# Optimization experiments

Hardware: AMD Instinct MI355X
Metric: run time of the kernel (lower is better)

Reference implementation:

```python
import jax, jax.numpy as jnp
import numpy as np
import math

ALPHA = 0.25
GAMMA = 2.0
STD = np.array([0.1, 0.1, 0.2, 0.2], dtype=np.float32).reshape(4, 1)


def setup_inputs() -> dict:
    rng = np.random.default_rng(0)
    B, C, Na, Nb = 8, 80, 49104, 64
    cls_pred = rng.uniform(0.01, 0.99, (B, C, Na)).astype(np.float32)
    reg_pred = (0.5 * rng.standard_normal((B, 4, Na))).astype(np.float32)
    # anchors in x1,y1,x2,y2 with positive width/height
    cx = rng.uniform(0.0, 512.0, Na); cy = rng.uniform(0.0, 512.0, Na)
    w = rng.uniform(16.0, 128.0, Na); h = rng.uniform(16.0, 128.0, Na)
    anchors = np.stack([cx - 0.5 * w, cy - 0.5 * h, cx + 0.5 * w, cy + 0.5 * h], 1).astype(np.float32)
    # annotations: valid boxes first, padded with label=-1
    x1 = rng.uniform(0.0, 380.0, (B, Nb)); y1 = rng.uniform(0.0, 380.0, (B, Nb))
    bw = rng.uniform(24.0, 120.0, (B, Nb)); bh = rng.uniform(24.0, 120.0, (B, Nb))
    lab = rng.integers(0, C, (B, Nb)).astype(np.float32)
    nvalid = rng.integers(1, Nb + 1, B)
    valid = np.arange(Nb)[None, :] < nvalid[:, None]
    lab = np.where(valid, lab, -1.0)
    annots = np.stack([x1, y1, x1 + bw, y1 + bh, lab], -1).astype(np.float32)
    return {"cls_pred": jnp.asarray(cls_pred), "reg_pred": jnp.asarray(reg_pred),
            "annots": jnp.asarray(annots), "anchors": jnp.asarray(anchors)}


def _focal(pred, targets):
    alpha_f = jnp.where(targets == 1.0, ALPHA, 1.0 - ALPHA)
    fw = jnp.where(targets == 1.0, 1.0 - pred, pred)
    bce = -(targets * jnp.log(pred) + (1.0 - targets) * jnp.log(1.0 - pred))
    return alpha_f * fw ** GAMMA * bce


def _ciou(acx, acy, aw, ah, gcx, gcy, gw, gh, reg):
    # acx/acy/aw/ah: [1,Na]; gt: [B,Na]; reg: [B,4,Na] (std-scaled)
    pcx = acx + reg[:, 0] * aw
    pcy = acy + reg[:, 1] * ah
    pw = jnp.exp(reg[:, 2]) * aw
    ph = jnp.exp(reg[:, 3]) * ah
    g_area = gw * gh
    p_area = pw * ph
    ix1 = jnp.maximum(gcx - 0.5 * gw, pcx - 0.5 * pw)
    ix2 = jnp.minimum(gcx + 0.5 * gw, pcx + 0.5 * pw)
    iy1 = jnp.maximum(gcy - 0.5 * gh, pcy - 0.5 * ph)
    iy2 = jnp.minimum(gcy + 0.5 * gh, pcy + 0.5 * ph)
    inter = jnp.clip(ix2 - ix1, 0.0) * jnp.clip(iy2 - iy1, 0.0)
    ex1 = jnp.minimum(gcx - 0.5 * gw, pcx - 0.5 * pw)
    ex2 = jnp.maximum(gcx + 0.5 * gw, pcx + 0.5 * pw)
    ey1 = jnp.minimum(gcy - 0.5 * gh, pcy - 0.5 * ph)
    ey2 = jnp.maximum(gcy + 0.5 * gh, pcy + 0.5 * ph)
    inter_diag = (gcx - pcx) ** 2 + (gcy - pcy) ** 2
    enc_diag = jnp.clip(ex2 - ex1, 0.0) ** 2 + jnp.clip(ey2 - ey1, 0.0) ** 2
    union = g_area + p_area - inter
    u = inter_diag / jnp.clip(enc_diag, 1e-6)
    iou = inter / jnp.clip(union, 1e-6)
    v = (4.0 / math.pi ** 2) * (jnp.arctan(gw / gh) - jnp.arctan(pw / ph)) ** 2
    S = (iou > 0.5).astype(iou.dtype)
    alpha = jax.lax.stop_gradient(S * v / jnp.clip(1.0 - iou + v, 1e-6))
    ciou = jnp.clip(iou - u - alpha * v, -1.0, 1.0)
    return 1.0 - ciou


def _multibox_loss(cls_pred, reg_pred, annots, anchors):
    reg = reg_pred * jnp.asarray(STD)[None]            # [B,4,Na]
    aw = anchors[:, 2] - anchors[:, 0]
    ah = anchors[:, 3] - anchors[:, 1]
    acx = anchors[:, 0] + 0.5 * aw
    acy = anchors[:, 1] + 0.5 * ah
    cls = jnp.clip(cls_pred, 1e-7, 1.0 - 1e-7)         # [B,C,Na]
    valid = annots[:, :, 4] != -1.0                    # [B,Nb]
    boxes = annots[:, :, :4]
    # dense IoU [B,Na,Nb]
    a = anchors[None, :, None, :]
    bx = boxes[:, None, :, :]
    a_area = aw * ah                                   # [Na]
    b_area = (boxes[..., 2] - boxes[..., 0]) * (boxes[..., 3] - boxes[..., 1])
    iw = jnp.clip(jnp.minimum(a[..., 2], bx[..., 2]) - jnp.maximum(a[..., 0], bx[..., 0]), 0.0)
    ih = jnp.clip(jnp.minimum(a[..., 3], bx[..., 3]) - jnp.maximum(a[..., 1], bx[..., 1]), 0.0)
    inter = iw * ih
    union = jnp.clip(a_area[None, :, None] + b_area[:, None, :] - inter, 1e-7)
    iou = inter / union
    iou = jnp.where(valid[:, None, :], iou, -1.0)      # mask padded boxes
    iou_max = iou.max(-1)                              # [B,Na]
    iou_arg = iou.argmax(-1)                           # [B,Na]
    has_boxes = valid.any(-1)                          # [B]
    pos = (iou_max >= 0.5) & has_boxes[:, None]        # [B,Na]
    assigned = jnp.take_along_axis(annots, iou_arg[..., None], axis=1)  # [B,Na,5]
    labels = assigned[..., 4].astype(jnp.int32)
    C = cls.shape[1]
    posf = pos.astype(cls.dtype)
    targets = jax.nn.one_hot(labels, C, dtype=cls.dtype) * posf[..., None]
    targets = jnp.transpose(targets, (0, 2, 1))        # [B,C,Na]
    num_pos = posf.sum(-1)                             # [B]
    cls_loss = _focal(cls, targets).sum((1, 2)) / jnp.clip(num_pos, 1.0)
    gw = jnp.clip(assigned[..., 2] - assigned[..., 0], 1.0)
    gh = jnp.clip(assigned[..., 3] - assigned[..., 1], 1.0)
    gcx = assigned[..., 0] + 0.5 * gw
    gcy = assigned[..., 1] + 0.5 * gh
    ciou = _ciou(acx[None], acy[None], aw[None], ah[None], gcx, gcy, gw, gh, reg)  # [B,Na]
    reg_loss = (ciou * posf).sum(-1) / jnp.clip(num_pos, 1.0)
    reg_loss = jnp.where(num_pos > 0, reg_loss, 0.0)
    return cls_loss.mean(), reg_loss.mean()


def reference(cls_pred, reg_pred, annots, anchors):
    return _multibox_loss(cls_pred, reg_pred, annots, anchors)
```

## Files before the change

### kernel.cpp

```cpp
#include <hip/hip_runtime.h>
#include <math.h>

#define NB_MAX 64
#define CCHUNK 10


__global__ __launch_bounds__(256) void assign_kernel(
    const float* __restrict__ reg_pred,
    const float* __restrict__ annots,
    const float* __restrict__ anchors,
    signed char* __restrict__ labels,
    float* __restrict__ reg_part,
    float* __restrict__ pos_part,
    int Na, int Nb, int nblkA)
{
    int b = blockIdx.y;
    int a = blockIdx.x * 256 + threadIdx.x;

    __shared__ float ann[NB_MAX][5];
    const float* ab = annots + b * Nb * 5;
    for (int i = threadIdx.x; i < Nb * 5; i += 256) ann[i / 5][i % 5] = ab[i];
    __syncthreads();

    float regv = 0.f, posv = 0.f;
    if (a < Na) {
        float4 anc = ((const float4*)anchors)[a];
        float ax1 = anc.x, ay1 = anc.y, ax2 = anc.z, ay2 = anc.w;
        float aw = ax2 - ax1, ah = ay2 - ay1;
        float a_area = aw * ah;

        float best = -1.f; int bestj = 0;
        for (int j = 0; j < Nb; ++j) {
            float lab = ann[j][4];
            float iou = -1.0f;
            if (lab != -1.0f) {
                float bx1 = ann[j][0], by1 = ann[j][1], bx2 = ann[j][2], by2 = ann[j][3];
                float iw = fmaxf(fminf(ax2, bx2) - fmaxf(ax1, bx1), 0.f);
                float ih = fmaxf(fminf(ay2, by2) - fmaxf(ay1, by1), 0.f);
                float inter = iw * ih;
                float b_area = (bx2 - bx1) * (by2 - by1);
                float un = fmaxf(a_area + b_area - inter, 1e-7f);
                iou = inter / un;
            }
            if (iou > best) { best = iou; bestj = j; }
        }

        signed char lout = -1;
        if (best >= 0.5f) {
            lout = (signed char)(int)ann[bestj][4];

            float r0 = reg_pred[(size_t)(b * 4 + 0) * Na + a] * 0.1f;
            float r1 = reg_pred[(size_t)(b * 4 + 1) * Na + a] * 0.1f;
            float r2 = reg_pred[(size_t)(b * 4 + 2) * Na + a] * 0.2f;
            float r3 = reg_pred[(size_t)(b * 4 + 3) * Na + a] * 0.2f;

            float acx = ax1 + 0.5f * aw, acy = ay1 + 0.5f * ah;
            float pcx = acx + r0 * aw;
            float pcy = acy + r1 * ah;
            float pw = expf(r2) * aw;
            float ph = expf(r3) * ah;

            float g0 = ann[bestj][0], g1 = ann[bestj][1];
            float g2 = ann[bestj][2], g3 = ann[bestj][3];
            float gw = fmaxf(g2 - g0, 1.0f);
            float gh = fmaxf(g3 - g1, 1.0f);
            float gcx = g0 + 0.5f * gw;
            float gcy = g1 + 0.5f * gh;

            float g_area = gw * gh, p_area = pw * ph;
            float ix1 = fmaxf(gcx - 0.5f * gw, pcx - 0.5f * pw);
            float ix2 = fminf(gcx + 0.5f * gw, pcx + 0.5f * pw);
            float iy1 = fmaxf(gcy - 0.5f * gh, pcy - 0.5f * ph);
            float iy2 = fminf(gcy + 0.5f * gh, pcy + 0.5f * ph);
            float inter = fmaxf(ix2 - ix1, 0.f) * fmaxf(iy2 - iy1, 0.f);

            float ex1 = fminf(gcx - 0.5f * gw, pcx - 0.5f * pw);
            float ex2 = fmaxf(gcx + 0.5f * gw, pcx + 0.5f * pw);
            float ey1 = fminf(gcy - 0.5f * gh, pcy - 0.5f * ph);
            float ey2 = fmaxf(gcy + 0.5f * gh, pcy + 0.5f * ph);

            float dx = gcx - pcx, dy = gcy - pcy;
            float inter_diag = dx * dx + dy * dy;
            float cdx = fmaxf(ex2 - ex1, 0.f), cdy = fmaxf(ey2 - ey1, 0.f);
            float enc_diag = cdx * cdx + cdy * cdy;

            float uni = g_area + p_area - inter;
            float u = inter_diag / fmaxf(enc_diag, 1e-6f);
            float iou = inter / fmaxf(uni, 1e-6f);
            float dv = atanf(gw / gh) - atanf(pw / ph);
            float v = (4.0f / (float)(M_PI * M_PI)) * dv * dv;
            float S = (iou > 0.5f) ? 1.f : 0.f;
            float alpha = S * v / fmaxf(1.f - iou + v, 1e-6f);
            float ciou = fminf(fmaxf(iou - u - alpha * v, -1.f), 1.f);
            regv = 1.f - ciou;
            posv = 1.f;
        }
        labels[(size_t)b * Na + a] = lout;
    }

    __shared__ float s1[4], s2[4];
    #pragma unroll
    for (int off = 32; off > 0; off >>= 1) {
        regv += __shfl_down(regv, off);
        posv += __shfl_down(posv, off);
    }
    int lane = threadIdx.x & 63, wid = threadIdx.x >> 6;
    if (lane == 0) { s1[wid] = regv; s2[wid] = posv; }
    __syncthreads();
    if (threadIdx.x == 0) {
        reg_part[(size_t)b * nblkA + blockIdx.x] = s1[0] + s1[1] + s1[2] + s1[3];
        pos_part[(size_t)b * nblkA + blockIdx.x] = s2[0] + s2[1] + s2[2] + s2[3];
    }
}

__device__ __forceinline__ float focal1(float p, bool t) {
    p = fminf(fmaxf(p, 1e-7f), 0.99999988f);
    float q = t ? p : 1.0f - p;
    float af = t ? 0.25f : 0.75f;
    float fw = 1.0f - q;
    return af * fw * fw * (-__logf(q));
}

__global__ __launch_bounds__(256) void focal_kernel(
    const float* __restrict__ cls_pred,
    const signed char* __restrict__ labels,
    float* __restrict__ cls_part,
    int Na, int C, int nchunk, int nblkF)
{
    int b = blockIdx.z;
    int No = Na >> 3;
    int Nq = Na >> 2;
    int q = blockIdx.x * 256 + threadIdx.x;
    int c0 = blockIdx.y * CCHUNK;
    int cend = min(c0 + CCHUNK, C);

    float sum = 0.f;
    if (q < No) {
        const char4* lp = (const char4*)(labels + (size_t)b * Na) + 2 * q;
        char4 la = lp[0], lb = lp[1];
        int l0 = la.x, l1 = la.y, l2 = la.z, l3 = la.w;
        int l4 = lb.x, l5 = lb.y, l6 = lb.z, l7 = lb.w;
        const float4* base = (const float4*)cls_pred + (size_t)b * C * Nq + 2 * q;
        for (int c = c0; c < cend; ++c) {
            float4 p0 = base[(size_t)c * Nq];
            float4 p1 = base[(size_t)c * Nq + 1];
            sum += focal1(p0.x, l0 == c);
            sum += focal1(p0.y, l1 == c);
            sum += focal1(p0.z, l2 == c);
            sum += focal1(p0.w, l3 == c);
            sum += focal1(p1.x, l4 == c);
            sum += focal1(p1.y, l5 == c);
            sum += focal1(p1.z, l6 == c);
            sum += focal1(p1.w, l7 == c);
        }
    }

    __shared__ float s[4];
    #pragma unroll
    for (int off = 32; off > 0; off >>= 1) sum += __shfl_down(sum, off);
    int lane = threadIdx.x & 63, wid = threadIdx.x >> 6;
    if (lane == 0) s[wid] = sum;
    __syncthreads();
    if (threadIdx.x == 0) {
        cls_part[(size_t)b * nblkF + blockIdx.x * nchunk + blockIdx.y] =
            s[0] + s[1] + s[2] + s[3];
    }
}

__global__ __launch_bounds__(512) void finalize_kernel(
    const float* __restrict__ reg_part,
    const float* __restrict__ pos_part,
    const float* __restrict__ cls_part,
    float* __restrict__ out,
    int B, int nblkA, int nblkF)
{
    int w = threadIdx.x >> 6;
    int lane = threadIdx.x & 63;

    float cs = 0.f, rs = 0.f, ps = 0.f;
    if (w < B) {
        for (int i = lane; i < nblkA; i += 64) {
            rs += reg_part[(size_t)w * nblkA + i];
            ps += pos_part[(size_t)w * nblkA + i];
        }
        for (int i = lane; i < nblkF; i += 64) {
            cs += cls_part[(size_t)w * nblkF + i];
        }
    }
    #pragma unroll
    for (int off = 32; off > 0; off >>= 1) {
        cs += __shfl_down(cs, off);
        rs += __shfl_down(rs, off);
        ps += __shfl_down(ps, off);
    }
    __shared__ float sc[8], sr[8];
    if (w < B && lane == 0) {
        float d = fmaxf(ps, 1.f);
        sc[w] = cs / d;
        sr[w] = (ps > 0.f) ? rs / d : 0.f;
    }
    __syncthreads();
    if (threadIdx.x == 0) {
        float a = 0.f, r = 0.f;
        for (int i = 0; i < B; ++i) { a += sc[i]; r += sr[i]; }
        out[0] = a / (float)B;
        out[1] = r / (float)B;
    }
}

extern "C" void kernel_launch(void* const* d_in, const int* in_sizes, int n_in,
                              void* d_out, int out_size, void* d_ws, size_t ws_size,
                              hipStream_t stream) {
    const float* cls     = (const float*)d_in[0];
    const float* reg     = (const float*)d_in[1];
    const float* annots  = (const float*)d_in[2];
    const float* anchors = (const float*)d_in[3];

    int Na = in_sizes[3] / 4;
    int B  = in_sizes[1] / (4 * Na);
    int C  = in_sizes[0] / (B * Na);
    int Nb = in_sizes[2] / (B * 5);

    int nblkA  = (Na + 255) / 256;
    int No     = Na / 8;
    int nblkX  = (No + 255) / 256;
    int nchunk = (C + CCHUNK - 1) / CCHUNK;
    int nblkF  = nblkX * nchunk;

    signed char* labels = (signed char*)d_ws;
    size_t off = ((size_t)B * Na + 255) & ~(size_t)255;
    float* reg_part = (float*)((char*)d_ws + off);
    float* pos_part = reg_part + (size_t)B * nblkA;
    float* cls_part = pos_part + (size_t)B * nblkA;
    float* out = (float*)d_out;

    dim3 g1(nblkA, B);
    assign_kernel<<<g1, 256, 0, stream>>>(reg, annots, anchors, labels,
                                          reg_part, pos_part, Na, Nb, nblkA);

    dim3 g2(nblkX, nchunk, B);
    focal_kernel<<<g2, 256, 0, stream>>>(cls, labels, cls_part, Na, C, nchunk, nblkF);

    finalize_kernel<<<1, 512, 0, stream>>>(reg_part, pos_part, cls_part, out,
                                           B, nblkA, nblkF);
}
```

Before: 210.7 us.

## Fuse anchor assignment and focal loss into a single kernel

Merges the assignment/CIoU kernel and the focal-loss kernel into one. Each thread handles two anchors, computes their labels in registers and then streams all C classes of cls_pred as float2. This removes the int8 label round-trip through global memory and one kernel launch. In exchange the grid shrinks to about 96 blocks per batch (about 770 total), each looping over all 80 classes. The Nb-long IoU search also runs serially before the memory-bound loop, which may lower occupancy and memory-level parallelism.

```diff
diff --git a/kernel.cpp b/kernel.cpp
--- a/kernel.cpp
+++ b/kernel.cpp
@@ -2,116 +2,7 @@
 #include <math.h>
 
 #define NB_MAX 64
-#define CCHUNK 10
-
-
-__global__ __launch_bounds__(256) void assign_kernel(
-    const float* __restrict__ reg_pred,
-    const float* __restrict__ annots,
-    const float* __restrict__ anchors,
-    signed char* __restrict__ labels,
-    float* __restrict__ reg_part,
-    float* __restrict__ pos_part,
-    int Na, int Nb, int nblkA)
-{
-    int b = blockIdx.y;
-    int a = blockIdx.x * 256 + threadIdx.x;
-
-    __shared__ float ann[NB_MAX][5];
-    const float* ab = annots + b * Nb * 5;
-    for (int i = threadIdx.x; i < Nb * 5; i += 256) ann[i / 5][i % 5] = ab[i];
-    __syncthreads();
-
-    float regv = 0.f, posv = 0.f;
-    if (a < Na) {
-        float4 anc = ((const float4*)anchors)[a];
-        float ax1 = anc.x, ay1 = anc.y, ax2 = anc.z, ay2 = anc.w;
-        float aw = ax2 - ax1, ah = ay2 - ay1;
-        float a_area = aw * ah;
-
-        float best = -1.f; int bestj = 0;
-        for (int j = 0; j < Nb; ++j) {
-            float lab = ann[j][4];
-            float iou = -1.0f;
-            if (lab != -1.0f) {
-                float bx1 = ann[j][0], by1 = ann[j][1], bx2 = ann[j][2], by2 = ann[j][3];
-                float iw = fmaxf(fminf(ax2, bx2) - fmaxf(ax1, bx1), 0.f);
-                float ih = fmaxf(fminf(ay2, by2) - fmaxf(ay1, by1), 0.f);
-                float inter = iw * ih;
-                float b_area = (bx2 - bx1) * (by2 - by1);
-                float un = fmaxf(a_area + b_area - inter, 1e-7f);
-                iou = inter / un;
-            }
-            if (iou > best) { best = iou; bestj = j; }
-        }
-
-        signed char lout = -1;
-        if (best >= 0.5f) {
-            lout = (signed char)(int)ann[bestj][4];
-
-            float r0 = reg_pred[(size_t)(b * 4 + 0) * Na + a] * 0.1f;
-            float r1 = reg_pred[(size_t)(b * 4 + 1) * Na + a] * 0.1f;
-            float r2 = reg_pred[(size_t)(b * 4 + 2) * Na + a] * 0.2f;
-            float r3 = reg_pred[(size_t)(b * 4 + 3) * Na + a] * 0.2f;
-
-            float acx = ax1 + 0.5f * aw, acy = ay1 + 0.5f * ah;
-            float pcx = acx + r0 * aw;
-            float pcy = acy + r1 * ah;
-            float pw = expf(r2) * aw;
-            float ph = expf(r3) * ah;
-
-            float g0 = ann[bestj][0], g1 = ann[bestj][1];
-            float g2 = ann[bestj][2], g3 = ann[bestj][3];
-            float gw = fmaxf(g2 - g0, 1.0f);
-            float gh = fmaxf(g3 - g1, 1.0f);
-            float gcx = g0 + 0.5f * gw;
-            float gcy = g1 + 0.5f * gh;
-
-            float g_area = gw * gh, p_area = pw * ph;
-            float ix1 = fmaxf(gcx - 0.5f * gw, pcx - 0.5f * pw);
-            float ix2 = fminf(gcx + 0.5f * gw, pcx + 0.5f * pw);
-            float iy1 = fmaxf(gcy - 0.5f * gh, pcy - 0.5f * ph);
-            float iy2 = fminf(gcy + 0.5f * gh, pcy + 0.5f * ph);
-            float inter = fmaxf(ix2 - ix1, 0.f) * fmaxf(iy2 - iy1, 0.f);
-
-            float ex1 = fminf(gcx - 0.5f * gw, pcx - 0.5f * pw);
-            float ex2 = fmaxf(gcx + 0.5f * gw, pcx + 0.5f * pw);
-            float ey1 = fminf(gcy - 0.5f * gh, pcy - 0.5f * ph);
-            float ey2 = fmaxf(gcy + 0.5f * gh, pcy + 0.5f * ph);
-
-            float dx = gcx - pcx, dy = gcy - pcy;
-            float inter_diag = dx * dx + dy * dy;
-            float cdx = fmaxf(ex2 - ex1, 0.f), cdy = fmaxf(ey2 - ey1, 0.f);
-            float enc_diag = cdx * cdx + cdy * cdy;
-
-            float uni = g_area + p_area - inter;
-            float u = inter_diag / fmaxf(enc_diag, 1e-6f);
-            float iou = inter / fmaxf(uni, 1e-6f);
-            float dv = atanf(gw / gh) - atanf(pw / ph);
-            float v = (4.0f / (float)(M_PI * M_PI)) * dv * dv;
-            float S = (iou > 0.5f) ? 1.f : 0.f;
-            float alpha = S * v / fmaxf(1.f - iou + v, 1e-6f);
-            float ciou = fminf(fmaxf(iou - u - alpha * v, -1.f), 1.f);
-            regv = 1.f - ciou;
-            posv = 1.f;
-        }
-        labels[(size_t)b * Na + a] = lout;
-    }
-
-    __shared__ float s1[4], s2[4];
-    #pragma unroll
-    for (int off = 32; off > 0; off >>= 1) {
-        regv += __shfl_down(regv, off);
-        posv += __shfl_down(posv, off);
-    }
-    int lane = threadIdx.x & 63, wid = threadIdx.x >> 6;
-    if (lane == 0) { s1[wid] = regv; s2[wid] = posv; }
-    __syncthreads();
-    if (threadIdx.x == 0) {
-        reg_part[(size_t)b * nblkA + blockIdx.x] = s1[0] + s1[1] + s1[2] + s1[3];
-        pos_part[(size_t)b * nblkA + blockIdx.x] = s2[0] + s2[1] + s2[2] + s2[3];
-    }
-}
+
 
 __device__ __forceinline__ float focal1(float p, bool t) {
     p = fminf(fmaxf(p, 1e-7f), 0.99999988f);
@@ -121,70 +12,149 @@
     return af * fw * fw * (-__logf(q));
 }
 
-__global__ __launch_bounds__(256) void focal_kernel(
+__global__ __launch_bounds__(256) void fused_kernel(
     const float* __restrict__ cls_pred,
-    const signed char* __restrict__ labels,
+    const float* __restrict__ reg_pred,
+    const float* __restrict__ annots,
+    const float* __restrict__ anchors,
     float* __restrict__ cls_part,
-    int Na, int C, int nchunk, int nblkF)
+    float* __restrict__ reg_part,
+    float* __restrict__ pos_part,
+    int Na, int Nb, int C, int nblk)
 {
-    int b = blockIdx.z;
-    int No = Na >> 3;
-    int Nq = Na >> 2;
-    int q = blockIdx.x * 256 + threadIdx.x;
-    int c0 = blockIdx.y * CCHUNK;
-    int cend = min(c0 + CCHUNK, C);
-
-    float sum = 0.f;
-    if (q < No) {
-        const char4* lp = (const char4*)(labels + (size_t)b * Na) + 2 * q;
-        char4 la = lp[0], lb = lp[1];
-        int l0 = la.x, l1 = la.y, l2 = la.z, l3 = la.w;
-        int l4 = lb.x, l5 = lb.y, l6 = lb.z, l7 = lb.w;
-        const float4* base = (const float4*)cls_pred + (size_t)b * C * Nq + 2 * q;
-        for (int c = c0; c < cend; ++c) {
-            float4 p0 = base[(size_t)c * Nq];
-            float4 p1 = base[(size_t)c * Nq + 1];
-            sum += focal1(p0.x, l0 == c);
-            sum += focal1(p0.y, l1 == c);
-            sum += focal1(p0.z, l2 == c);
-            sum += focal1(p0.w, l3 == c);
-            sum += focal1(p1.x, l4 == c);
-            sum += focal1(p1.y, l5 == c);
-            sum += focal1(p1.z, l6 == c);
-            sum += focal1(p1.w, l7 == c);
+    int b = blockIdx.y;
+    int h = blockIdx.x * 256 + threadIdx.x;
+    int Nh = Na >> 1;
+
+    __shared__ float ann[NB_MAX][5];
+    const float* ab = annots + b * Nb * 5;
+    for (int i = threadIdx.x; i < Nb * 5; i += 256) ann[i / 5][i % 5] = ab[i];
+    __syncthreads();
+
+    float clsv = 0.f, regv = 0.f, posv = 0.f;
+    int lab[2] = {-1, -1};
+
+    if (h < Nh) {
+        #pragma unroll
+        for (int s = 0; s < 2; ++s) {
+            int a = 2 * h + s;
+            float4 anc = ((const float4*)anchors)[a];
+            float ax1 = anc.x, ay1 = anc.y, ax2 = anc.z, ay2 = anc.w;
+            float aw = ax2 - ax1, ah = ay2 - ay1;
+            float a_area = aw * ah;
+
+            float best = -1.f; int bestj = 0;
+            for (int j = 0; j < Nb; ++j) {
+                float labj = ann[j][4];
+                float iou = -1.0f;
+                if (labj != -1.0f) {
+                    float bx1 = ann[j][0], by1 = ann[j][1];
+                    float bx2 = ann[j][2], by2 = ann[j][3];
+                    float iw = fmaxf(fminf(ax2, bx2) - fmaxf(ax1, bx1), 0.f);
+                    float ih = fmaxf(fminf(ay2, by2) - fmaxf(ay1, by1), 0.f);
+                    float inter = iw * ih;
+                    float b_area = (bx2 - bx1) * (by2 - by1);
+                    float un = fmaxf(a_area + b_area - inter, 1e-7f);
+                    iou = inter / un;
+                }
+                if (iou > best) { best = iou; bestj = j; }
+            }
+
+            if (best >= 0.5f) {
+                lab[s] = (int)ann[bestj][4];
+
+                float r0 = reg_pred[(size_t)(b * 4 + 0) * Na + a] * 0.1f;
+                float r1 = reg_pred[(size_t)(b * 4 + 1) * Na + a] * 0.1f;
+                float r2 = reg_pred[(size_t)(b * 4 + 2) * Na + a] * 0.2f;
+                float r3 = reg_pred[(size_t)(b * 4 + 3) * Na + a] * 0.2f;
+
+                float acx = ax1 + 0.5f * aw, acy = ay1 + 0.5f * ah;
+                float pcx = acx + r0 * aw;
+                float pcy = acy + r1 * ah;
+                float pw = expf(r2) * aw;
+                float ph = expf(r3) * ah;
+
+                float g0 = ann[bestj][0], g1 = ann[bestj][1];
+                float g2 = ann[bestj][2], g3 = ann[bestj][3];
+                float gw = fmaxf(g2 - g0, 1.0f);
+                float gh = fmaxf(g3 - g1, 1.0f);
+                float gcx = g0 + 0.5f * gw;
+                float gcy = g1 + 0.5f * gh;
+
+                float g_area = gw * gh, p_area = pw * ph;
+                float ix1 = fmaxf(gcx - 0.5f * gw, pcx - 0.5f * pw);
+                float ix2 = fminf(gcx + 0.5f * gw, pcx + 0.5f * pw);
+                float iy1 = fmaxf(gcy - 0.5f * gh, pcy - 0.5f * ph);
+                float iy2 = fminf(gcy + 0.5f * gh, pcy + 0.5f * ph);
+                float inter = fmaxf(ix2 - ix1, 0.f) * fmaxf(iy2 - iy1, 0.f);
+
+                float ex1 = fminf(gcx - 0.5f * gw, pcx - 0.5f * pw);
+                float ex2 = fmaxf(gcx + 0.5f * gw, pcx + 0.5f * pw);
+                float ey1 = fminf(gcy - 0.5f * gh, pcy - 0.5f * ph);
+                float ey2 = fmaxf(gcy + 0.5f * gh, pcy + 0.5f * ph);
+
+                float dx = gcx - pcx, dy = gcy - pcy;
+                float inter_diag = dx * dx + dy * dy;
+                float cdx = fmaxf(ex2 - ex1, 0.f), cdy = fmaxf(ey2 - ey1, 0.f);
+                float enc_diag = cdx * cdx + cdy * cdy;
+
+                float uni = g_area + p_area - inter;
+                float u = inter_diag / fmaxf(enc_diag, 1e-6f);
+                float iou = inter / fmaxf(uni, 1e-6f);
+                float dv = atanf(gw / gh) - atanf(pw / ph);
+                float v = (4.0f / (float)(M_PI * M_PI)) * dv * dv;
+                float S = (iou > 0.5f) ? 1.f : 0.f;
+                float alpha = S * v / fmaxf(1.f - iou + v, 1e-6f);
+                float ciou = fminf(fmaxf(iou - u - alpha * v, -1.f), 1.f);
+                regv += 1.f - ciou;
+                posv += 1.f;
+            }
         }
-    }
-
-    __shared__ float s[4];
+
+        int l0 = lab[0], l1 = lab[1];
+        const float2* base = (const float2*)cls_pred + (size_t)b * C * Nh + h;
+        #pragma unroll 4
+        for (int c = 0; c < C; ++c) {
+            float2 p = base[(size_t)c * Nh];
+            clsv += focal1(p.x, l0 == c);
+            clsv += focal1(p.y, l1 == c);
+        }
+    }
+
+    __shared__ float s1[4], s2[4], s3[4];
     #pragma unroll
-    for (int off = 32; off > 0; off >>= 1) sum += __shfl_down(sum, off);
+    for (int off = 32; off > 0; off >>= 1) {
+        clsv += __shfl_down(clsv, off);
+        regv += __shfl_down(regv, off);
+        posv += __shfl_down(posv, off);
+    }
     int lane = threadIdx.x & 63, wid = threadIdx.x >> 6;
-    if (lane == 0) s[wid] = sum;
+    if (lane == 0) { s1[wid] = clsv; s2[wid] = regv; s3[wid] = posv; }
     __syncthreads();
     if (threadIdx.x == 0) {
-        cls_part[(size_t)b * nblkF + blockIdx.x * nchunk + blockIdx.y] =
-            s[0] + s[1] + s[2] + s[3];
+        size_t slot = (size_t)b * nblk + blockIdx.x;
+        cls_part[slot] = s1[0] + s1[1] + s1[2] + s1[3];
+        reg_part[slot] = s2[0] + s2[1] + s2[2] + s2[3];
+        pos_part[slot] = s3[0] + s3[1] + s3[2] + s3[3];
     }
 }
 
 __global__ __launch_bounds__(512) void finalize_kernel(
+    const float* __restrict__ cls_part,
     const float* __restrict__ reg_part,
     const float* __restrict__ pos_part,
-    const float* __restrict__ cls_part,
     float* __restrict__ out,
-    int B, int nblkA, int nblkF)
+    int B, int nblk)
 {
     int w = threadIdx.x >> 6;
     int lane = threadIdx.x & 63;
 
     float cs = 0.f, rs = 0.f, ps = 0.f;
     if (w < B) {
-        for (int i = lane; i < nblkA; i += 64) {
-            rs += reg_part[(size_t)w * nblkA + i];
-            ps += pos_part[(size_t)w * nblkA + i];
-        }
-        for (int i = lane; i < nblkF; i += 64) {
-            cs += cls_part[(size_t)w * nblkF + i];
+        for (int i = lane; i < nblk; i += 64) {
+            cs += cls_part[(size_t)w * nblk + i];
+            rs += reg_part[(size_t)w * nblk + i];
+            ps += pos_part[(size_t)w * nblk + i];
         }
     }
     #pragma unroll
@@ -221,26 +191,19 @@
     int C  = in_sizes[0] / (B * Na);
     int Nb = in_sizes[2] / (B * 5);
 
-    int nblkA  = (Na + 255) / 256;
-    int No     = Na / 8;
-    int nblkX  = (No + 255) / 256;
-    int nchunk = (C + CCHUNK - 1) / CCHUNK;
-    int nblkF  = nblkX * nchunk;
-
-    signed char* labels = (signed char*)d_ws;
-    size_t off = ((size_t)B * Na + 255) & ~(size_t)255;
-    float* reg_part = (float*)((char*)d_ws + off);
-    float* pos_part = reg_part + (size_t)B * nblkA;
-    float* cls_part = pos_part + (size_t)B * nblkA;
+    int Nh   = Na / 2;
+    int nblk = (Nh + 255) / 256;
+
+    float* cls_part = (float*)d_ws;
+    float* reg_part = cls_part + (size_t)B * nblk;
+    float* pos_part = reg_part + (size_t)B * nblk;
     float* out = (float*)d_out;
 
-    dim3 g1(nblkA, B);
-    assign_kernel<<<g1, 256, 0, stream>>>(reg, annots, anchors, labels,
-                                          reg_part, pos_part, Na, Nb, nblkA);
-
-    dim3 g2(nblkX, nchunk, B);
-    focal_kernel<<<g2, 256, 0, stream>>>(cls, labels, cls_part, Na, C, nchunk, nblkF);
-
-    finalize_kernel<<<1, 512, 0, stream>>>(reg_part, pos_part, cls_part, out,
-                                           B, nblkA, nblkF);
-}
+    dim3 g1(nblk, B);
+    fused_kernel<<<g1, 256, 0, stream>>>(cls, reg, annots, anchors,
+                                         cls_part, reg_part, pos_part,
+                                         Na, Nb, C, nblk);
+
+    finalize_kernel<<<1, 512, 0, stream>>>(cls_part, reg_part, pos_part, out,
+                                           B, nblk);
+}
```

Measured after the change: 205.2 us. 1.03x faster.

## Restructure focal kernel to one class row per block with 4 independent loads

Applied to the files above, without the earlier changes.

The focal kernel now gives each block one (batch, class) row segment of 4096 anchors, with every thread issuing four independent float4 loads and the matching label char4 loads up front. It replaces the earlier per-thread loop over a 10-class chunk. The aim is more memory-level parallelism and a simpler grid for the bandwidth-bound pass over cls_pred, at the cost of reloading the labels once per class. The assignment loop also stops at the first padded annotation instead of checking every slot, which relies on valid boxes being stored first.

```diff
diff --git a/kernel.cpp b/kernel.cpp
--- a/kernel.cpp
+++ b/kernel.cpp
@@ -2,7 +2,6 @@
 #include <math.h>
 
 #define NB_MAX 64
-#define CCHUNK 10
 
 
 __global__ __launch_bounds__(256) void assign_kernel(
@@ -31,17 +30,15 @@
 
         float best = -1.f; int bestj = 0;
         for (int j = 0; j < Nb; ++j) {
-            float lab = ann[j][4];
-            float iou = -1.0f;
-            if (lab != -1.0f) {
-                float bx1 = ann[j][0], by1 = ann[j][1], bx2 = ann[j][2], by2 = ann[j][3];
-                float iw = fmaxf(fminf(ax2, bx2) - fmaxf(ax1, bx1), 0.f);
-                float ih = fmaxf(fminf(ay2, by2) - fmaxf(ay1, by1), 0.f);
-                float inter = iw * ih;
-                float b_area = (bx2 - bx1) * (by2 - by1);
-                float un = fmaxf(a_area + b_area - inter, 1e-7f);
-                iou = inter / un;
-            }
+            float labj = ann[j][4];
+            if (labj == -1.0f) break;
+            float bx1 = ann[j][0], by1 = ann[j][1], bx2 = ann[j][2], by2 = ann[j][3];
+            float iw = fmaxf(fminf(ax2, bx2) - fmaxf(ax1, bx1), 0.f);
+            float ih = fmaxf(fminf(ay2, by2) - fmaxf(ay1, by1), 0.f);
+            float inter = iw * ih;
+            float b_area = (bx2 - bx1) * (by2 - by1);
+            float un = fmaxf(a_area + b_area - inter, 1e-7f);
+            float iou = inter / un;
             if (iou > best) { best = iou; bestj = j; }
         }
 
@@ -121,37 +118,46 @@
     return af * fw * fw * (-__logf(q));
 }
 
+__device__ __forceinline__ float focal4(float4 p, char4 l, int c) {
+    return focal1(p.x, l.x == c) + focal1(p.y, l.y == c) +
+           focal1(p.z, l.z == c) + focal1(p.w, l.w == c);
+}
+
 __global__ __launch_bounds__(256) void focal_kernel(
     const float* __restrict__ cls_pred,
     const signed char* __restrict__ labels,
     float* __restrict__ cls_part,
-    int Na, int C, int nchunk, int nblkF)
+    int Na, int C, int nseg)
 {
-    int b = blockIdx.z;
-    int No = Na >> 3;
+    int b = blockIdx.z, c = blockIdx.y;
     int Nq = Na >> 2;
-    int q = blockIdx.x * 256 + threadIdx.x;
-    int c0 = blockIdx.y * CCHUNK;
-    int cend = min(c0 + CCHUNK, C);
+    int q = blockIdx.x * 1024 + threadIdx.x;
+    const float4* row = (const float4*)cls_pred + ((size_t)b * C + c) * Nq;
+    const char4* labr = (const char4*)labels + (size_t)b * Nq;
 
     float sum = 0.f;
-    if (q < No) {
-        const char4* lp = (const char4*)(labels + (size_t)b * Na) + 2 * q;
-        char4 la = lp[0], lb = lp[1];
-        int l0 = la.x, l1 = la.y, l2 = la.z, l3 = la.w;
-        int l4 = lb.x, l5 = lb.y, l6 = lb.z, l7 = lb.w;
-        const float4* base = (const float4*)cls_pred + (size_t)b * C * Nq + 2 * q;
-        for (int c = c0; c < cend; ++c) {
-            float4 p0 = base[(size_t)c * Nq];
-            float4 p1 = base[(size_t)c * Nq + 1];
-            sum += focal1(p0.x, l0 == c);
-            sum += focal1(p0.y, l1 == c);
-            sum += focal1(p0.z, l2 == c);
-            sum += focal1(p0.w, l3 == c);
-            sum += focal1(p1.x, l4 == c);
-            sum += focal1(p1.y, l5 == c);
-            sum += focal1(p1.z, l6 == c);
-            sum += focal1(p1.w, l7 == c);
+    if (blockIdx.x + 1 < nseg) {
+        float4 pA = row[q];
+        float4 pB = row[q + 256];
+        float4 pC = row[q + 512];
+        float4 pD = row[q + 768];
+        char4 lA = labr[q];
+        char4 lB = labr[q + 256];
+        char4 lC = labr[q + 512];
+        char4 lD = labr[q + 768];
+        sum  = focal4(pA, lA, c);
+        sum += focal4(pB, lB, c);
+        sum += focal4(pC, lC, c);
+        sum += focal4(pD, lD, c);
+    } else {
+        #pragma unroll
+        for (int u = 0; u < 4; ++u) {
+            int qq = q + u * 256;
+            if (qq < Nq) {
+                float4 p = row[qq];
+                char4 l = labr[qq];
+                sum += focal4(p, l, c);
+            }
         }
     }
 
@@ -162,17 +168,16 @@
     if (lane == 0) s[wid] = sum;
     __syncthreads();
     if (threadIdx.x == 0) {
-        cls_part[(size_t)b * nblkF + blockIdx.x * nchunk + blockIdx.y] =
-            s[0] + s[1] + s[2] + s[3];
+        cls_part[((size_t)b * C + c) * nseg + blockIdx.x] = s[0] + s[1] + s[2] + s[3];
     }
 }
 
 __global__ __launch_bounds__(512) void finalize_kernel(
+    const float* __restrict__ cls_part,
     const float* __restrict__ reg_part,
     const float* __restrict__ pos_part,
-    const float* __restrict__ cls_part,
     float* __restrict__ out,
-    int B, int nblkA, int nblkF)
+    int B, int nblkA, int nC)
 {
     int w = threadIdx.x >> 6;
     int lane = threadIdx.x & 63;
@@ -183,8 +188,8 @@
             rs += reg_part[(size_t)w * nblkA + i];
             ps += pos_part[(size_t)w * nblkA + i];
         }
-        for (int i = lane; i < nblkF; i += 64) {
-            cs += cls_part[(size_t)w * nblkF + i];
+        for (int i = lane; i < nC; i += 64) {
+            cs += cls_part[(size_t)w * nC + i];
         }
     }
     #pragma unroll
@@ -221,14 +226,13 @@
     int C  = in_sizes[0] / (B * Na);
     int Nb = in_sizes[2] / (B * 5);
 
-    int nblkA  = (Na + 255) / 256;
-    int No     = Na / 8;
-    int nblkX  = (No + 255) / 256;
-    int nchunk = (C + CCHUNK - 1) / CCHUNK;
-    int nblkF  = nblkX * nchunk;
+    int nblkA = (Na + 255) / 256;
+    int Nq    = Na / 4;
+    int nseg  = (Nq + 1023) / 1024;
+    int nC    = C * nseg;
 
     signed char* labels = (signed char*)d_ws;
-    size_t off = ((size_t)B * Na + 255) & ~(size_t)255;
+    size_t off = (((size_t)B * Na) + 255) & ~(size_t)255;
     float* reg_part = (float*)((char*)d_ws + off);
     float* pos_part = reg_part + (size_t)B * nblkA;
     float* cls_part = pos_part + (size_t)B * nblkA;
@@ -238,9 +242,9 @@
     assign_kernel<<<g1, 256, 0, stream>>>(reg, annots, anchors, labels,
                                           reg_part, pos_part, Na, Nb, nblkA);
 
-    dim3 g2(nblkX, nchunk, B);
-    focal_kernel<<<g2, 256, 0, stream>>>(cls, labels, cls_part, Na, C, nchunk, nblkF);
-
-    finalize_kernel<<<1, 512, 0, stream>>>(reg_part, pos_part, cls_part, out,
-                                           B, nblkA, nblkF);
-}
+    dim3 g2(nseg, C, B);
+    focal_kernel<<<g2, 256, 0, stream>>>(cls, labels, cls_part, Na, C, nseg);
+
+    finalize_kernel<<<1, 512, 0, stream>>>(cls_part, reg_part, pos_part, out,
+                                           B, nblkA, nC);
+}
```

Result: no change. 211.5 us (+0.4%).
